# Kernel optimization log

Measured on AMD Instinct MI355X. Metric: run time of the kernel, lower is better.

Reference implementation:

```python
import jax, jax.numpy as jnp
import numpy as np

NUM_FEATS = 100000
EMB_DIM = 64
ATT_DIM = 64


def setup_inputs() -> dict:
    key = jax.random.key(0)
    ks = jax.random.split(key, 9)
    B, F = 2048, 39
    feat_index = jax.random.randint(ks[0], (B, F), 0, NUM_FEATS)
    feat_value = jax.random.uniform(ks[1], (B, F), dtype=jnp.float32)
    # parameters
    fo_w = jax.random.normal(ks[2], (NUM_FEATS, 1), dtype=jnp.float32) * 0.01
    emb_table = jax.random.normal(ks[3], (NUM_FEATS, EMB_DIM), dtype=jnp.float32) * 0.01
    att_W = jax.random.normal(ks[4], (EMB_DIM, ATT_DIM), dtype=jnp.float32) * (1.0 / np.sqrt(EMB_DIM))
    att_b = jax.random.normal(ks[5], (ATT_DIM,), dtype=jnp.float32)
    att_h = jax.random.normal(ks[6], (ATT_DIM,), dtype=jnp.float32)
    p_vec = jax.random.normal(ks[7], (EMB_DIM,), dtype=jnp.float32)
    bias = jax.random.normal(ks[8], (), dtype=jnp.float32)
    return {"feat_index": feat_index, "feat_value": feat_value, "fo_w": fo_w,
            "emb_table": emb_table, "att_W": att_W, "att_b": att_b,
            "att_h": att_h, "p_vec": p_vec, "bias": bias}


def _cross_indices(num_fields):
    row, col = np.triu_indices(num_fields, k=1)
    return jnp.asarray(row), jnp.asarray(col)


def reference(feat_index, feat_value, fo_w, emb_table, att_W, att_b, att_h, p_vec, bias):
    B, F = feat_index.shape
    fv = feat_value[:, :, None]                      # [B,F,1]
    # first-order term
    y_first = jnp.sum(fo_w[feat_index] * fv, axis=1)[:, 0]   # [B]
    # embeddings scaled by values
    feat_emb = emb_table[feat_index] * fv            # [B,F,D]
    row, col = _cross_indices(F)
    inter = feat_emb[:, row] * feat_emb[:, col]      # [B,P,D], P=F*(F-1)/2
    # location-based attention
    sig = jax.nn.relu(jnp.einsum('bpd,da->bpa', inter, att_W) + att_b)
    sig = jnp.sum(sig * att_h, axis=2)               # [B,P]
    att = jax.nn.softmax(sig, axis=1)                # [B,P]
    pooled = jnp.einsum('bp,bpd->bd', att, inter)    # [B,D]
    att_pool = jnp.sum(pooled * p_vec, axis=1)       # [B]
    y = jax.nn.sigmoid(bias + y_first + att_pool)    # [B]
    return y
```

## Files before the change

kernel.cpp:

```cpp
#include <hip/hip_runtime.h>
#include <hip/hip_fp16.h>

#define NUM_F  39
#define NUM_P  741
#define NPAD   768
#define DIM    64
#define ESTRH  72
#define NRP    2
#define NITEMS (2 * NUM_F * 8)

typedef float    f32x4 __attribute__((ext_vector_type(4)));
typedef _Float16 f16x8 __attribute__((ext_vector_type(8)));

static __device__ __forceinline__ f16x8 pack8(float4 v0, float4 v1, float fv) {
    f16x8 hv;
    hv[0] = (_Float16)(v0.x * fv);
    hv[1] = (_Float16)(v0.y * fv);
    hv[2] = (_Float16)(v0.z * fv);
    hv[3] = (_Float16)(v0.w * fv);
    hv[4] = (_Float16)(v1.x * fv);
    hv[5] = (_Float16)(v1.y * fv);
    hv[6] = (_Float16)(v1.z * fv);
    hv[7] = (_Float16)(v1.w * fv);
    return hv;
}

__global__ __launch_bounds__(512, 4) void afm_pp(
    const int*   __restrict__ feat_index,
    const float* __restrict__ feat_value,
    const float* __restrict__ fo_w,
    const float* __restrict__ emb_table,
    const float* __restrict__ att_W,
    const float* __restrict__ att_b,
    const float* __restrict__ att_h,
    const float* __restrict__ p_vec,
    const float* __restrict__ bias,
    float*       __restrict__ out)
{
    const int blk  = blockIdx.x;
    const int t    = threadIdx.x;
    const int wave = t >> 6;
    const int lane = t & 63;
    const int row  = wave >> 2;
    const int wv   = wave & 3;
    const int la   = lane & 15;
    const int lg   = lane >> 4;

    __shared__ __half       e_lds[2][2][NUM_F][ESTRH];
    __shared__ __half       Wt[DIM][ESTRH];
    __shared__ float2       sq_s[2][NPAD];
    __shared__ float        b_lds[DIM], h_lds[DIM], pv_lds[DIM];
    __shared__ unsigned int pairOff[NPAD];
    __shared__ int          s_idx[2 * NRP * NUM_F];
    __shared__ float        s_fv[2 * NRP * NUM_F];
    __shared__ float        yf_s[2 * NRP * NUM_F];
    __shared__ float        s_yfirst[2 * NRP];
    __shared__ float        wredM[8], wredS[8], wredQ[8];

    const float4* emb4 = (const float4*)emb_table;

    if (t < 2 * NRP * NUM_F) {
        int   idx = feat_index[blk * 2 * NRP * NUM_F + t];
        float fv  = feat_value[blk * 2 * NRP * NUM_F + t];
        s_idx[t]  = idx;
        s_fv[t]   = fv;
        yf_s[t]   = fo_w[idx] * fv;
    }
    if (t < DIM) {
        b_lds[t]  = att_b[t];
        h_lds[t]  = att_h[t];
        pv_lds[t] = p_vec[t];
    }
    if (t >= 192 && t < 192 + NUM_F) {
        int r = t - 192, off = r * (2 * NUM_F - r - 1) / 2;
        const unsigned int rb = (unsigned int)(r * (ESTRH * 2));
        for (int c = r + 1; c < NUM_F; ++c) {
            pairOff[off] = rb | ((unsigned int)(c * (ESTRH * 2)) << 16);
            ++off;
        }
    }
    if (t >= 256 && t < 256 + (NPAD - NUM_P)) pairOff[NUM_P + (t - 256)] = 0;
    for (int q = t; q < DIM * DIM; q += 512) {
        int d = q >> 6, a = q & 63;
        Wt[a][d] = (__half)(_Float16)att_W[q];
    }
    __syncthreads();

    if (wave < 2 * NRP) {
        float yf = (lane < NUM_F) ? yf_s[wave * NUM_F + lane] : 0.f;
        #pragma unroll
        for (int m = 1; m < 64; m <<= 1) yf += __shfl_xor(yf, m);
        if (lane == 0) s_yfirst[wave] = yf;
    }

    {
        const int f0 = t >> 3, d80 = t & 7;
        float4 v0a = emb4[(size_t)s_idx[f0] * 16 + d80 * 2];
        float4 v0b = emb4[(size_t)s_idx[f0] * 16 + d80 * 2 + 1];
        const int  i1   = t + 512;
        const bool has1 = i1 < NITEMS;
        const int  f1 = i1 >> 3, d81 = i1 & 7;
        float4 v1a, v1b;
        if (has1) {
            v1a = emb4[(size_t)s_idx[f1] * 16 + d81 * 2];
            v1b = emb4[(size_t)s_idx[f1] * 16 + d81 * 2 + 1];
        }
        {
            int rr = (f0 >= NUM_F), ff = f0 - rr * NUM_F;
            *(f16x8*)&e_lds[0][rr][ff][d80 * 8] = pack8(v0a, v0b, s_fv[f0]);
        }
        if (has1) {
            int rr = (f1 >= NUM_F), ff = f1 - rr * NUM_F;
            *(f16x8*)&e_lds[0][rr][ff][d81 * 8] = pack8(v1a, v1b, s_fv[f1]);
        }
    }
    __syncthreads();

    const f16x8 WA00 = *(const f16x8*)&Wt[ 0 + la][ 0 + lg * 8];
    const f16x8 WA01 = *(const f16x8*)&Wt[ 0 + la][32 + lg * 8];
    const f16x8 WA10 = *(const f16x8*)&Wt[16 + la][ 0 + lg * 8];
    const f16x8 WA11 = *(const f16x8*)&Wt[16 + la][32 + lg * 8];
    const f16x8 WA20 = *(const f16x8*)&Wt[32 + la][ 0 + lg * 8];
    const f16x8 WA21 = *(const f16x8*)&Wt[32 + la][32 + lg * 8];
    const f16x8 WA30 = *(const f16x8*)&Wt[48 + la][ 0 + lg * 8];
    const f16x8 WA31 = *(const f16x8*)&Wt[48 + la][32 + lg * 8];

    f16x8 PA0 = (f16x8)(_Float16)0.f;
    f16x8 PA1 = (f16x8)(_Float16)0.f;
    if (la == 0) {
        #pragma unroll
        for (int j = 0; j < 8; ++j) {
            PA0[j] = (_Float16)pv_lds[     lg * 8 + j];
            PA1[j] = (_Float16)pv_lds[32 + lg * 8 + j];
        }
    }

    const f32x4 b40 = *(const f32x4*)&b_lds[ 0 + lg * 4];
    const f32x4 b41 = *(const f32x4*)&b_lds[16 + lg * 4];
    const f32x4 b42 = *(const f32x4*)&b_lds[32 + lg * 4];
    const f32x4 b43 = *(const f32x4*)&b_lds[48 + lg * 4];
    const f32x4 h40 = *(const f32x4*)&h_lds[ 0 + lg * 4];
    const f32x4 h41 = *(const f32x4*)&h_lds[16 + lg * 4];
    const f32x4 h42 = *(const f32x4*)&h_lds[32 + lg * 4];
    const f32x4 h43 = *(const f32x4*)&h_lds[48 + lg * 4];
    const f32x4 z4  = {0.f, 0.f, 0.f, 0.f};

    const int lgo = lg * 16;

    for (int rp = 0; rp < NRP; ++rp) {
        float4 n0a, n0b, n1a, n1b;
        int    nf0 = 0, nd0 = 0, nf1 = 0, nd1 = 0;
        bool   nhas1 = false;
        if (rp + 1 < NRP) {
            const int off = (rp + 1) * 2 * NUM_F;
            nf0 = t >> 3; nd0 = t & 7;
            n0a = emb4[(size_t)s_idx[off + nf0] * 16 + nd0 * 2];
            n0b = emb4[(size_t)s_idx[off + nf0] * 16 + nd0 * 2 + 1];
            const int i1 = t + 512;
            nhas1 = i1 < NITEMS;
            nf1 = i1 >> 3; nd1 = i1 & 7;
            if (nhas1) {
                n1a = emb4[(size_t)s_idx[off + nf1] * 16 + nd1 * 2];
                n1b = emb4[(size_t)s_idx[off + nf1] * 16 + nd1 * 2 + 1];
            }
        }

        const char* e_base = (const char*)&e_lds[rp & 1][row][0][0];

        #pragma unroll 1
        for (int it = 0; it < 12; ++it) {
            const int tile = wv + it * 4;
            const int p    = (tile << 4) + la;
            const unsigned rc = pairOff[p];
            const unsigned ro = rc & 0xFFFFu;
            const unsigned co = rc >> 16;

            const f16x8 er0 = *(const f16x8*)(e_base + ro + lgo);
            const f16x8 er1 = *(const f16x8*)(e_base + ro + lgo + 64);
            const f16x8 ec0 = *(const f16x8*)(e_base + co + lgo);
            const f16x8 ec1 = *(const f16x8*)(e_base + co + lgo + 64);
            const f16x8 B0 = er0 * ec0;
            const f16x8 B1 = er1 * ec1;

            __builtin_amdgcn_s_setprio(1);
            f32x4 a0 = __builtin_amdgcn_mfma_f32_16x16x32_f16(WA00, B0, b40, 0, 0, 0);
            f32x4 a1 = __builtin_amdgcn_mfma_f32_16x16x32_f16(WA10, B0, b41, 0, 0, 0);
            f32x4 a2 = __builtin_amdgcn_mfma_f32_16x16x32_f16(WA20, B0, b42, 0, 0, 0);
            f32x4 a3 = __builtin_amdgcn_mfma_f32_16x16x32_f16(WA30, B0, b43, 0, 0, 0);
            f32x4 aq = __builtin_amdgcn_mfma_f32_16x16x32_f16(PA0,  B0, z4,  0, 0, 0);
            a0 = __builtin_amdgcn_mfma_f32_16x16x32_f16(WA01, B1, a0, 0, 0, 0);
            a1 = __builtin_amdgcn_mfma_f32_16x16x32_f16(WA11, B1, a1, 0, 0, 0);
            a2 = __builtin_amdgcn_mfma_f32_16x16x32_f16(WA21, B1, a2, 0, 0, 0);
            a3 = __builtin_amdgcn_mfma_f32_16x16x32_f16(WA31, B1, a3, 0, 0, 0);
            aq = __builtin_amdgcn_mfma_f32_16x16x32_f16(PA1,  B1, aq, 0, 0, 0);
            __builtin_amdgcn_s_setprio(0);

            float s0 = fmaxf(a0[0], 0.f) * h40[0];
            float s1 = fmaxf(a1[0], 0.f) * h41[0];
            float s2 = fmaxf(a2[0], 0.f) * h42[0];
            float s3 = fmaxf(a3[0], 0.f) * h43[0];
            s0 = fmaf(fmaxf(a0[1], 0.f), h40[1], s0);
            s1 = fmaf(fmaxf(a1[1], 0.f), h41[1], s1);
            s2 = fmaf(fmaxf(a2[1], 0.f), h42[1], s2);
            s3 = fmaf(fmaxf(a3[1], 0.f), h43[1], s3);
            s0 = fmaf(fmaxf(a0[2], 0.f), h40[2], s0);
            s1 = fmaf(fmaxf(a1[2], 0.f), h41[2], s1);
            s2 = fmaf(fmaxf(a2[2], 0.f), h42[2], s2);
            s3 = fmaf(fmaxf(a3[2], 0.f), h43[2], s3);
            s0 = fmaf(fmaxf(a0[3], 0.f), h40[3], s0);
            s1 = fmaf(fmaxf(a1[3], 0.f), h41[3], s1);
            s2 = fmaf(fmaxf(a2[3], 0.f), h42[3], s2);
            s3 = fmaf(fmaxf(a3[3], 0.f), h43[3], s3);
            float ts = (s0 + s1) + (s2 + s3);
            ts += __shfl_xor(ts, 16);
            ts += __shfl_xor(ts, 32);

            if (lg == 0 && p < NUM_P) {
                sq_s[row][p] = make_float2(ts, aq[0]);
            }
        }
        __syncthreads();

        const int t2 = wv * 64 + lane;
        float sv0, sv1, sv2, qv0, qv1, qv2;
        {
            float2 x0 = sq_s[row][t2];
            float2 x1 = sq_s[row][t2 + 256];
            bool ok2 = (t2 + 512) < NUM_P;
            float2 x2 = ok2 ? sq_s[row][t2 + 512] : make_float2(-1e30f, 0.f);
            sv0 = x0.x; qv0 = x0.y;
            sv1 = x1.x; qv1 = x1.y;
            sv2 = x2.x; qv2 = x2.y;
            if (t2 + 256 >= NUM_P) { sv1 = -1e30f; qv1 = 0.f; }
            if (t2 >= NUM_P)       { sv0 = -1e30f; qv0 = 0.f; }
        }

        float m3 = fmaxf(fmaxf(sv0, sv1), sv2);
        #pragma unroll
        for (int mm = 1; mm < 64; mm <<= 1) m3 = fmaxf(m3, __shfl_xor(m3, mm));
        if (lane == 0) wredM[wave] = m3;
        __syncthreads();
        const int r4 = row * 4;
        const float M = fmaxf(fmaxf(wredM[r4 + 0], wredM[r4 + 1]),
                              fmaxf(wredM[r4 + 2], wredM[r4 + 3]));

        float e0 = __expf(sv0 - M);
        float e1 = __expf(sv1 - M);
        float e2 = __expf(sv2 - M);
        float S  = e0 + e1 + e2;
        float Q  = fmaf(e0, qv0, fmaf(e1, qv1, e2 * qv2));
        #pragma unroll
        for (int mm = 1; mm < 64; mm <<= 1) {
            S += __shfl_xor(S, mm);
            Q += __shfl_xor(Q, mm);
        }
        if (lane == 0) { wredS[wave] = S; wredQ[wave] = Q; }
        __syncthreads();

        if (lane == 0 && wv == 0) {
            const float Ssum = wredS[r4] + wredS[r4 + 1] + wredS[r4 + 2] + wredS[r4 + 3];
            const float Qsum = wredQ[r4] + wredQ[r4 + 1] + wredQ[r4 + 2] + wredQ[r4 + 3];
            const float att_pool = Qsum / Ssum;
            const float x = bias[0] + s_yfirst[rp * 2 + row] + att_pool;
            out[blk * (2 * NRP) + rp * 2 + row] = 1.f / (1.f + __expf(-x));
        }

        if (rp + 1 < NRP) {
            const int off = (rp + 1) * 2 * NUM_F;
            {
                int rr = (nf0 >= NUM_F), ff = nf0 - rr * NUM_F;
                *(f16x8*)&e_lds[(rp + 1) & 1][rr][ff][nd0 * 8] =
                    pack8(n0a, n0b, s_fv[off + nf0]);
            }
            if (nhas1) {
                int rr = (nf1 >= NUM_F), ff = nf1 - rr * NUM_F;
                *(f16x8*)&e_lds[(rp + 1) & 1][rr][ff][nd1 * 8] =
                    pack8(n1a, n1b, s_fv[off + nf1]);
            }
            __syncthreads();
        }
    }
}

extern "C" void kernel_launch(void* const* d_in, const int* in_sizes, int n_in,
                              void* d_out, int out_size, void* d_ws, size_t ws_size,
                              hipStream_t stream) {
    const int*   feat_index = (const int*)  d_in[0];
    const float* feat_value = (const float*)d_in[1];
    const float* fo_w       = (const float*)d_in[2];
    const float* emb_table  = (const float*)d_in[3];
    const float* att_W      = (const float*)d_in[4];
    const float* att_b      = (const float*)d_in[5];
    const float* att_h      = (const float*)d_in[6];
    const float* p_vec      = (const float*)d_in[7];
    const float* bias       = (const float*)d_in[8];
    float*       out        = (float*)d_out;

    const int B = in_sizes[0] / NUM_F;

    afm_pp<<<B / (2 * NRP), 512, 0, stream>>>(feat_index, feat_value, fo_w, emb_table,
                                              att_W, att_b, att_h, p_vec, bias, out);
}
```

Measured before the change: 29.38 us.

## Compute pair indices analytically and replace shuffle reduction with LDS partials

Drops the precomputed pairOff LDS table and derives the (row, col) field pair for each pair index with a closed-form sqrt formula. Removes the two cross-lane shuffles per tile: each lane group now writes its partial attention score to a 4-way LDS array, and the softmax stage sums the four partials. Launch bounds are relaxed from 4 to 2 blocks per CU, which allows more registers per thread. The trade-off is more LDS writes and reads, extra ALU work for sqrt, more shared memory that may lower occupancy, and a float sqrt that could misindex a pair from rounding.

```diff
diff --git a/kernel.cpp b/kernel.cpp
--- a/kernel.cpp
+++ b/kernel.cpp
@@ -25,7 +25,7 @@
     return hv;
 }
 
-__global__ __launch_bounds__(512, 4) void afm_pp(
+__global__ __launch_bounds__(512, 2) void afm_nsh(
     const int*   __restrict__ feat_index,
     const float* __restrict__ feat_value,
     const float* __restrict__ fo_w,
@@ -46,16 +46,16 @@
     const int la   = lane & 15;
     const int lg   = lane >> 4;
 
-    __shared__ __half       e_lds[2][2][NUM_F][ESTRH];
-    __shared__ __half       Wt[DIM][ESTRH];
-    __shared__ float2       sq_s[2][NPAD];
-    __shared__ float        b_lds[DIM], h_lds[DIM], pv_lds[DIM];
-    __shared__ unsigned int pairOff[NPAD];
-    __shared__ int          s_idx[2 * NRP * NUM_F];
-    __shared__ float        s_fv[2 * NRP * NUM_F];
-    __shared__ float        yf_s[2 * NRP * NUM_F];
-    __shared__ float        s_yfirst[2 * NRP];
-    __shared__ float        wredM[8], wredS[8], wredQ[8];
+    __shared__ __half  e_lds[2][2][NUM_F][ESTRH];
+    __shared__ __half  Wt[DIM][ESTRH];
+    __shared__ float   tsp[2][4][NPAD];
+    __shared__ float   q_s[2][NPAD];
+    __shared__ float   b_lds[DIM], h_lds[DIM], pv_lds[DIM];
+    __shared__ int     s_idx[2 * NRP * NUM_F];
+    __shared__ float   s_fv[2 * NRP * NUM_F];
+    __shared__ float   yf_s[2 * NRP * NUM_F];
+    __shared__ float   s_yfirst[2 * NRP];
+    __shared__ float   wredM[8], wredS[8], wredQ[8];
 
     const float4* emb4 = (const float4*)emb_table;
 
@@ -71,15 +71,6 @@
         h_lds[t]  = att_h[t];
         pv_lds[t] = p_vec[t];
     }
-    if (t >= 192 && t < 192 + NUM_F) {
-        int r = t - 192, off = r * (2 * NUM_F - r - 1) / 2;
-        const unsigned int rb = (unsigned int)(r * (ESTRH * 2));
-        for (int c = r + 1; c < NUM_F; ++c) {
-            pairOff[off] = rb | ((unsigned int)(c * (ESTRH * 2)) << 16);
-            ++off;
-        }
-    }
-    if (t >= 256 && t < 256 + (NPAD - NUM_P)) pairOff[NUM_P + (t - 256)] = 0;
     for (int q = t; q < DIM * DIM; q += 512) {
         int d = q >> 6, a = q & 63;
         Wt[a][d] = (__half)(_Float16)att_W[q];
@@ -171,9 +162,13 @@
         for (int it = 0; it < 12; ++it) {
             const int tile = wv + it * 4;
             const int p    = (tile << 4) + la;
-            const unsigned rc = pairOff[p];
-            const unsigned ro = rc & 0xFFFFu;
-            const unsigned co = rc >> 16;
+            const int pc   = (p < NUM_P - 1) ? p : (NUM_P - 1);
+
+            const float disc = (float)(5929 - 8 * pc);
+            const int r  = (int)((77.0f - sqrtf(disc)) * 0.5f);
+            const int c  = pc - ((r * (77 - r)) >> 1) + r + 1;
+            const int ro = r * (ESTRH * 2);
+            const int co = c * (ESTRH * 2);
 
             const f16x8 er0 = *(const f16x8*)(e_base + ro + lgo);
             const f16x8 er1 = *(const f16x8*)(e_base + ro + lgo + 64);
@@ -211,26 +206,26 @@
             s1 = fmaf(fmaxf(a1[3], 0.f), h41[3], s1);
             s2 = fmaf(fmaxf(a2[3], 0.f), h42[3], s2);
             s3 = fmaf(fmaxf(a3[3], 0.f), h43[3], s3);
-            float ts = (s0 + s1) + (s2 + s3);
-            ts += __shfl_xor(ts, 16);
-            ts += __shfl_xor(ts, 32);
-
-            if (lg == 0 && p < NUM_P) {
-                sq_s[row][p] = make_float2(ts, aq[0]);
-            }
+            const float ts = (s0 + s1) + (s2 + s3);
+
+            tsp[row][lg][p] = ts;
+            if (lg == 0) q_s[row][p] = aq[0];
         }
         __syncthreads();
 
         const int t2 = wv * 64 + lane;
         float sv0, sv1, sv2, qv0, qv1, qv2;
         {
-            float2 x0 = sq_s[row][t2];
-            float2 x1 = sq_s[row][t2 + 256];
-            bool ok2 = (t2 + 512) < NUM_P;
-            float2 x2 = ok2 ? sq_s[row][t2 + 512] : make_float2(-1e30f, 0.f);
-            sv0 = x0.x; qv0 = x0.y;
-            sv1 = x1.x; qv1 = x1.y;
-            sv2 = x2.x; qv2 = x2.y;
+            sv0 = tsp[row][0][t2] + tsp[row][1][t2]
+                + tsp[row][2][t2] + tsp[row][3][t2];
+            qv0 = q_s[row][t2];
+            sv1 = tsp[row][0][t2 + 256] + tsp[row][1][t2 + 256]
+                + tsp[row][2][t2 + 256] + tsp[row][3][t2 + 256];
+            qv1 = q_s[row][t2 + 256];
+            const bool ok2 = (t2 + 512) < NUM_P;
+            sv2 = ok2 ? (tsp[row][0][t2 + 512] + tsp[row][1][t2 + 512]
+                       + tsp[row][2][t2 + 512] + tsp[row][3][t2 + 512]) : -1e30f;
+            qv2 = ok2 ? q_s[row][t2 + 512] : 0.f;
             if (t2 + 256 >= NUM_P) { sv1 = -1e30f; qv1 = 0.f; }
             if (t2 >= NUM_P)       { sv0 = -1e30f; qv0 = 0.f; }
         }
@@ -298,6 +293,6 @@
 
     const int B = in_sizes[0] / NUM_F;
 
-    afm_pp<<<B / (2 * NRP), 512, 0, stream>>>(feat_index, feat_value, fo_w, emb_table,
-                                              att_W, att_b, att_h, p_vec, bias, out);
+    afm_nsh<<<B / (2 * NRP), 512, 0, stream>>>(feat_index, feat_value, fo_w, emb_table,
+                                               att_W, att_b, att_h, p_vec, bias, out);
 }
```

Result: slower. 36.57 us (+24.5%).
